# Kernel optimization log

Measured on AMD Instinct MI355X. Metric: run time of the kernel, lower is better.

The kernel has to match this reference:

```python
import jax, jax.numpy as jnp
import numpy as np

LN_EPS = 1e-5


def setup_inputs() -> dict:
    key = jax.random.key(0)
    ks = jax.random.split(key, 5)
    B, L, D, H = 4, 4096, 2048, 16
    s = 0.02  # keep activations in a sane range for fp32
    return {
        "x": jax.random.normal(ks[0], (B, L, D), jnp.float32),
        "Wq": jax.random.normal(ks[1], (D, D), jnp.float32) * s,
        "Wv": jax.random.normal(ks[2], (D, D), jnp.float32) * s,
        "Wg": jax.random.normal(ks[3], (D, D), jnp.float32) * s,
        "Wo": jax.random.normal(ks[4], (D, D), jnp.float32) * s,
        "beta": jnp.full((H,), -0.2, jnp.float32),  # module init: _beta = -0.2
        "ln_w": jnp.ones((D,), jnp.float32),
        "ln_b": jnp.zeros((D,), jnp.float32),
    }


def _retention_scan(v, lam):
    # v: (B, L, H, Dh); lam: (H,). state_t = lam * state_{t-1} + v_t
    B, L, H, Dh = v.shape
    a = jnp.broadcast_to(lam[None, None, :, None], (B, L, H, 1))

    def combine(c1, c2):
        a1, b1 = c1
        a2, b2 = c2
        return (a1 * a2, b1 * a2 + b2)

    _, state = jax.lax.associative_scan(combine, (a, v), axis=1)
    return state  # (B, L, H, Dh)


def reference(x, Wq, Wv, Wg, Wo, beta, ln_w, ln_b):
    B, L, D = x.shape
    H = beta.shape[0]
    Dh = D // H
    # bias-free projections (torch Linear: x @ W.T)
    q = (x @ Wq.T).reshape(B, L, H, Dh)
    v = (x @ Wv.T).reshape(B, L, H, Dh)
    lam = jax.nn.sigmoid(beta)  # per-head decay, (H,)
    state = _retention_scan(v, lam)  # decay-weighted cumulative sum
    y = (q * state).reshape(B, L, D)
    # LayerNorm over d_model
    mu = jnp.mean(y, axis=-1, keepdims=True)
    var = jnp.mean(jnp.square(y - mu), axis=-1, keepdims=True)
    y = (y - mu) * jax.lax.rsqrt(var + LN_EPS) * ln_w + ln_b
    # SiLU gate
    y = y * jax.nn.silu(x @ Wg.T)
    return y @ Wo.T
```

## Files before the change

kernel.cpp:

```cpp
#include <hip/hip_runtime.h>

#define BATCH 4
#define SEQ   4096
#define DMODEL 2048
#define NHEAD 16
#define DHEAD 128
#define MROWS (BATCH*SEQ)
#define LC    128
#define NCH   (SEQ/LC)

typedef unsigned short ushort_t;
typedef __bf16 v8bf __attribute__((ext_vector_type(8)));
typedef float  f32x4 __attribute__((ext_vector_type(4)));

__device__ __forceinline__ float b2f(ushort_t h) {
    return __uint_as_float(((unsigned)h) << 16);
}
__device__ __forceinline__ ushort_t f2b(float f) {
    unsigned u = __float_as_uint(f);
    return (ushort_t)((u + 0x7fffu + ((u >> 16) & 1u)) >> 16);
}

__global__ void cast_f32_bf16(const float* __restrict__ in, ushort_t* __restrict__ out, int n) {
    int i = (blockIdx.x * blockDim.x + threadIdx.x) * 8;
    const int stride = gridDim.x * blockDim.x * 8;
    for (; i < n; i += stride) {
        float4 a = *(const float4*)(in + i);
        float4 b = *(const float4*)(in + i + 4);
        ushort_t o[8] = {f2b(a.x), f2b(a.y), f2b(a.z), f2b(a.w),
                         f2b(b.x), f2b(b.y), f2b(b.z), f2b(b.w)};
        *(uint4*)(out + i) = *(const uint4*)o;
    }
}

__global__ void cast_weights(const float* __restrict__ w0, const float* __restrict__ w1,
                             const float* __restrict__ w2, const float* __restrict__ w3,
                             ushort_t* __restrict__ o0, ushort_t* __restrict__ o1,
                             ushort_t* __restrict__ o2, ushort_t* __restrict__ o3) {
    const int wsel = blockIdx.y;
    const float* src = wsel == 0 ? w0 : wsel == 1 ? w1 : wsel == 2 ? w2 : w3;
    ushort_t* dst    = wsel == 0 ? o0 : wsel == 1 ? o1 : wsel == 2 ? o2 : o3;
    const int n = DMODEL * DMODEL;
    int i = (blockIdx.x * blockDim.x + threadIdx.x) * 8;
    const int stride = gridDim.x * blockDim.x * 8;
    for (; i < n; i += stride) {
        float4 a = *(const float4*)(src + i);
        float4 b = *(const float4*)(src + i + 4);
        ushort_t o[8] = {f2b(a.x), f2b(a.y), f2b(a.z), f2b(a.w),
                         f2b(b.x), f2b(b.y), f2b(b.z), f2b(b.w)};
        *(uint4*)(dst + i) = *(const uint4*)o;
    }
}


#define GLL(src, dstoff) __builtin_amdgcn_global_load_lds( \
    (const __attribute__((address_space(1))) void*)(src), \
    (__attribute__((address_space(3))) void*)((char*)lds + (dstoff)), 16, 0, 0)

#define STG_A(buf, ks, kt) do { \
    GLL(gA0 + (kt) + (ks) * 32, (buf) * 65536 + (ks) * 16384 + dst0); \
    GLL(gA1 + (kt) + (ks) * 32, (buf) * 65536 + (ks) * 16384 + dst1); } while (0)
#define STG_B(buf, ks, kt) do { \
    GLL(gB0 + (kt) + (ks) * 32, (buf) * 65536 + 32768 + (ks) * 16384 + dst0); \
    GLL(gB1 + (kt) + (ks) * 32, (buf) * 65536 + 32768 + (ks) * 16384 + dst1); } while (0)

#define DSA(buf, ks, mh) do { \
    const ushort_t* _p = lds + (buf) * 32768 + (ks) * 8192 + abase + (mh) * 2048; \
    abuf[0] = *(const v8bf*)_p;          abuf[1] = *(const v8bf*)(_p + 512); \
    abuf[2] = *(const v8bf*)(_p + 1024); abuf[3] = *(const v8bf*)(_p + 1536); } while (0)
#define DSB(buf, ks) do { \
    const ushort_t* _p = lds + (buf) * 32768 + (ks) * 8192 + bbase; \
    bbuf[0] = *(const v8bf*)_p;          bbuf[1] = *(const v8bf*)(_p + 512); \
    bbuf[2] = *(const v8bf*)(_p + 1024); bbuf[3] = *(const v8bf*)(_p + 1536); } while (0)

#define VMW(n) asm volatile("s_waitcnt vmcnt(" #n ")" ::: "memory")
#define BAR()  __builtin_amdgcn_s_barrier()

#define MFMA_CORE(mh) do { \
    __builtin_amdgcn_s_barrier(); \
    asm volatile("s_waitcnt lgkmcnt(0)" ::: "memory"); \
    __builtin_amdgcn_sched_barrier(0); \
    __builtin_amdgcn_s_setprio(1); \
    _Pragma("unroll") \
    for (int _m = 0; _m < 4; ++_m) \
        _Pragma("unroll") \
        for (int _n = 0; _n < 4; ++_n) \
            acc[(mh) * 4 + _m][_n] = __builtin_amdgcn_mfma_f32_16x16x32_bf16( \
                abuf[_m], bbuf[_n], acc[(mh) * 4 + _m][_n], 0, 0, 0); \
    __builtin_amdgcn_s_setprio(0); \
    __builtin_amdgcn_sched_barrier(0); \
} while (0)

template<int N, int EPI>
__global__ __launch_bounds__(512, 2) void gemm8(const ushort_t* __restrict__ A,
                                                const ushort_t* __restrict__ Bm,
                                                ushort_t* __restrict__ o0,
                                                ushort_t* __restrict__ o1,
                                                ushort_t* __restrict__ o2,
                                                float* __restrict__ of) {
    constexpr int K  = DMODEL;
    constexpr int NT = K / 64;
    constexpr int NBN = N / 256;
    constexpr int NWG = (MROWS / 256) * NBN;
    extern __shared__ ushort_t lds[];

    int wg = blockIdx.x;
    wg = (wg & 7) * (NWG / 8) + (wg >> 3);
    const int tm = (wg / NBN) * 256;
    const int tn = (wg % NBN) * 256;

    const int tid  = threadIdx.x;
    const int lane = tid & 63;
    const int wid  = tid >> 6;
    const int wr   = wid >> 2;
    const int wc   = wid & 3;

    const int s0  = wid * 128 + lane;
    const int s1  = s0 + 64;
    const int r0s = s0 >> 2, r1s = s1 >> 2;
    const int c0s = (s0 & 3) ^ (r0s & 3) ^ ((r0s >> 2) & 3);
    const int c1s = (s1 & 3) ^ (r1s & 3) ^ ((r1s >> 2) & 3);
    const ushort_t* gA0 = A  + (size_t)(tm + r0s) * K + c0s * 8;
    const ushort_t* gA1 = A  + (size_t)(tm + r1s) * K + c1s * 8;
    const ushort_t* gB0 = Bm + (size_t)(tn + r0s) * K + c0s * 8;
    const ushort_t* gB1 = Bm + (size_t)(tn + r1s) * K + c1s * 8;
    const int dst0 = wid * 2048;
    const int dst1 = dst0 + 1024;

    const int l4    = lane & 15;
    const int c16p  = (lane >> 4) ^ (lane & 3) ^ ((lane >> 2) & 3);
    const int abase = (wr * 128 + l4) * 32 + c16p * 8;
    const int bbase = 16384 + (wc * 64 + l4) * 32 + c16p * 8;

    f32x4 acc[8][4] = {};
    v8bf abuf[4], bbuf[4];

    STG_A(0, 0, 0); STG_B(0, 0, 0); STG_A(0, 1, 0); STG_B(0, 1, 0);
    VMW(4);
    BAR();

    for (int t = 0; t < NT - 1; ++t) {
        const int cur = t & 1, nxt = cur ^ 1;
        const int ktn = (t + 1) * 64;
        STG_A(nxt, 0, ktn);
        DSA(cur, 0, 0); DSB(cur, 0);
        MFMA_CORE(0);
        BAR();
        STG_B(nxt, 0, ktn);
        DSA(cur, 0, 1);
        MFMA_CORE(1);
        VMW(4);
        BAR();
        STG_A(nxt, 1, ktn);
        DSA(cur, 1, 0); DSB(cur, 1);
        MFMA_CORE(0);
        BAR();
        STG_B(nxt, 1, ktn);
        DSA(cur, 1, 1);
        MFMA_CORE(1);
        VMW(4);
        BAR();
    }
    {
        const int cur = (NT - 1) & 1;
        DSA(cur, 0, 0); DSB(cur, 0);
        MFMA_CORE(0);
        BAR();
        DSA(cur, 0, 1);
        MFMA_CORE(1);
        VMW(0);
        BAR();
        DSA(cur, 1, 0); DSB(cur, 1);
        MFMA_CORE(0);
        BAR();
        DSA(cur, 1, 1);
        MFMA_CORE(1);
    }

    const int cr = (lane >> 4) * 4;
    const int cc = lane & 15;
    if constexpr (EPI == 0) {
        ushort_t* out = (tn < 2048) ? o0 : (tn < 4096 ? o1 : o2);
        const int nc0 = tn & 2047;
#pragma unroll
        for (int m = 0; m < 8; ++m) {
            const int r0 = tm + wr * 128 + m * 16 + cr;
#pragma unroll
            for (int n = 0; n < 4; ++n) {
                const int c = nc0 + wc * 64 + n * 16 + cc;
#pragma unroll
                for (int j = 0; j < 4; ++j)
                    out[(size_t)(r0 + j) * 2048 + c] = f2b(acc[m][n][j]);
            }
        }
    } else {
#pragma unroll
        for (int m = 0; m < 8; ++m) {
            const int r0 = tm + wr * 128 + m * 16 + cr;
#pragma unroll
            for (int n = 0; n < 4; ++n) {
                const int c = tn + wc * 64 + n * 16 + cc;
#pragma unroll
                for (int j = 0; j < 4; ++j)
                    of[(size_t)(r0 + j) * N + c] = acc[m][n][j];
            }
        }
    }
}

__global__ void scan_pass1(const ushort_t* __restrict__ v, const float* __restrict__ beta,
                           float* __restrict__ cf) {
    const int chunk = blockIdx.x, h = blockIdx.y, b = blockIdx.z;
    const int dh = threadIdx.x;
    const float lam = 1.f / (1.f + __expf(-beta[h]));
    size_t idx = ((size_t)(b * SEQ + chunk * LC) * NHEAD + h) * DHEAD + dh;
    float s = 0.f;
#pragma unroll 4
    for (int l = 0; l < LC; ++l) {
        s = fmaf(s, lam, b2f(v[idx]));
        idx += DMODEL;
    }
    cf[(((size_t)(b * NHEAD + h) * NCH) + chunk) * DHEAD + dh] = s;
}

__global__ void scan_pass2(float* __restrict__ cf, const float* __restrict__ beta) {
    const int t = blockIdx.x * blockDim.x + threadIdx.x;
    const int dh = t & 127;
    const int bh = t >> 7;
    const int h = bh & 15;
    const float lam = 1.f / (1.f + __expf(-beta[h]));
    float lamLc = lam;
#pragma unroll
    for (int i = 0; i < 7; ++i) lamLc *= lamLc;
    float carry = 0.f;
    for (int c = 0; c < NCH; ++c) {
        const size_t i = ((size_t)bh * NCH + c) * DHEAD + dh;
        const float val = cf[i];
        cf[i] = carry;
        carry = fmaf(carry, lamLc, val);
    }
}

__global__ void scan_pass3(const ushort_t* __restrict__ v, const ushort_t* __restrict__ q,
                           const float* __restrict__ beta, const float* __restrict__ cf,
                           ushort_t* __restrict__ y) {
    const int chunk = blockIdx.x, h = blockIdx.y, b = blockIdx.z;
    const int dh = threadIdx.x;
    const float lam = 1.f / (1.f + __expf(-beta[h]));
    float s = cf[(((size_t)(b * NHEAD + h) * NCH) + chunk) * DHEAD + dh];
    size_t idx = ((size_t)(b * SEQ + chunk * LC) * NHEAD + h) * DHEAD + dh;
#pragma unroll 4
    for (int l = 0; l < LC; ++l) {
        s = fmaf(s, lam, b2f(v[idx]));
        y[idx] = f2b(b2f(q[idx]) * s);
        idx += DMODEL;
    }
}

__global__ __launch_bounds__(256) void ln_gate(const ushort_t* __restrict__ y,
                                               const ushort_t* g,
                                               const float* __restrict__ lnw,
                                               const float* __restrict__ lnb,
                                               ushort_t* t) {
    const int row = blockIdx.x;
    const int tid = threadIdx.x;
    const size_t base = (size_t)row * DMODEL + tid * 8;

    float yv[8];
    {
        const uint4 raw = *(const uint4*)(y + base);
        const ushort_t* p = (const ushort_t*)&raw;
#pragma unroll
        for (int j = 0; j < 8; ++j) yv[j] = b2f(p[j]);
    }
    float s = 0.f, ss = 0.f;
#pragma unroll
    for (int j = 0; j < 8; ++j) { s += yv[j]; ss += yv[j] * yv[j]; }

#pragma unroll
    for (int o = 32; o > 0; o >>= 1) { s += __shfl_down(s, o); ss += __shfl_down(ss, o); }
    __shared__ float red[8];
    const int wid = tid >> 6, lane = tid & 63;
    if (lane == 0) { red[wid] = s; red[4 + wid] = ss; }
    __syncthreads();
    s  = red[0] + red[1] + red[2] + red[3];
    ss = red[4] + red[5] + red[6] + red[7];

    const float mu = s * (1.f / DMODEL);
    const float var = ss * (1.f / DMODEL) - mu * mu;
    const float rs = rsqrtf(var + 1e-5f);

    const int c0 = tid * 8;
    float4 w0 = *(const float4*)(lnw + c0), w1 = *(const float4*)(lnw + c0 + 4);
    float4 b0 = *(const float4*)(lnb + c0), b1 = *(const float4*)(lnb + c0 + 4);
    const float wv[8] = {w0.x, w0.y, w0.z, w0.w, w1.x, w1.y, w1.z, w1.w};
    const float bv[8] = {b0.x, b0.y, b0.z, b0.w, b1.x, b1.y, b1.z, b1.w};

    float gv[8];
    {
        const uint4 raw = *(const uint4*)(g + base);
        const ushort_t* p = (const ushort_t*)&raw;
#pragma unroll
        for (int j = 0; j < 8; ++j) gv[j] = b2f(p[j]);
    }

    ushort_t out[8];
#pragma unroll
    for (int j = 0; j < 8; ++j) {
        const float tv = (yv[j] - mu) * rs * wv[j] + bv[j];
        const float sil = gv[j] / (1.f + __expf(-gv[j]));
        out[j] = f2b(tv * sil);
    }
    *(uint4*)(t + base) = *(const uint4*)out;
}

#define OFF_XB  ((size_t)0)
#define OFF_WC  (OFF_XB + (size_t)MROWS*DMODEL*2)
#define OFF_WOB (OFF_WC + (size_t)3*DMODEL*DMODEL*2)
#define OFF_G   (OFF_WOB + (size_t)DMODEL*DMODEL*2)
#define OFF_CF  (OFF_G + (size_t)MROWS*DMODEL*2)
#define OFF_END (OFF_CF + (size_t)BATCH*NHEAD*NCH*DHEAD*4)

extern "C" void kernel_launch(void* const* d_in, const int* in_sizes, int n_in,
                              void* d_out, int out_size, void* d_ws, size_t ws_size,
                              hipStream_t stream) {
    if (ws_size < OFF_END) return;

    const float* x    = (const float*)d_in[0];
    const float* Wq   = (const float*)d_in[1];
    const float* Wv   = (const float*)d_in[2];
    const float* Wg   = (const float*)d_in[3];
    const float* Wo   = (const float*)d_in[4];
    const float* beta = (const float*)d_in[5];
    const float* lnw  = (const float*)d_in[6];
    const float* lnb  = (const float*)d_in[7];

    char* ws = (char*)d_ws;
    ushort_t* xb  = (ushort_t*)(ws + OFF_XB);
    ushort_t* Wc  = (ushort_t*)(ws + OFF_WC);
    ushort_t* Wob = (ushort_t*)(ws + OFF_WOB);
    ushort_t* g   = (ushort_t*)(ws + OFF_G);
    float*    cf  = (float*)(ws + OFF_CF);

    ushort_t* q = (ushort_t*)d_out;
    ushort_t* v = q + (size_t)MROWS * DMODEL;
    ushort_t* y = xb;
    ushort_t* t = g;

    const int DD = DMODEL * DMODEL;

    (void)hipFuncSetAttribute((const void*)gemm8<3 * DMODEL, 0>,
                              hipFuncAttributeMaxDynamicSharedMemorySize, 131072);
    (void)hipFuncSetAttribute((const void*)gemm8<DMODEL, 1>,
                              hipFuncAttributeMaxDynamicSharedMemorySize, 131072);

    cast_f32_bf16<<<2048, 256, 0, stream>>>(x, xb, MROWS * DMODEL);
    cast_weights<<<dim3(256, 4), 256, 0, stream>>>(Wq, Wv, Wg, Wo,
                                                   Wc, Wc + DD, Wc + 2 * DD, Wob);

    gemm8<3 * DMODEL, 0><<<(MROWS / 256) * (3 * DMODEL / 256), 512, 131072, stream>>>(
        xb, Wc, q, v, g, nullptr);

    scan_pass1<<<dim3(NCH, NHEAD, BATCH), DHEAD, 0, stream>>>(v, beta, cf);
    scan_pass2<<<(BATCH * NHEAD * DHEAD) / 256, 256, 0, stream>>>(cf, beta);
    scan_pass3<<<dim3(NCH, NHEAD, BATCH), DHEAD, 0, stream>>>(v, q, beta, cf, y);

    ln_gate<<<MROWS, 256, 0, stream>>>(y, g, lnw, lnb, t);

    gemm8<DMODEL, 1><<<(MROWS / 256) * (DMODEL / 256), 512, 131072, stream>>>(
        t, Wob, nullptr, nullptr, nullptr, (float*)d_out);
}
```

Baseline: 681.8 us.

## Restructure GEMM LDS layout to 64-wide rows and cut barriers per k-tile

Changes the LDS staging layout from two 32-column sub-slabs to full 64-column rows with an 8-way XOR swizzle, and rewrites the global-to-LDS load addressing to match. The main loop now waits on vmcnt and barriers once per k-tile at the start instead of at every MFMA quarter, which removes most workgroup barriers. Loads for the next buffer are issued between the four MFMA quarters. This relies on the vmcnt accounting being right for the double buffer, and it changes the bank-conflict pattern of the LDS reads.

```diff
diff --git a/kernel.cpp b/kernel.cpp
--- a/kernel.cpp
+++ b/kernel.cpp
@@ -57,27 +57,26 @@
     (const __attribute__((address_space(1))) void*)(src), \
     (__attribute__((address_space(3))) void*)((char*)lds + (dstoff)), 16, 0, 0)
 
-#define STG_A(buf, ks, kt) do { \
-    GLL(gA0 + (kt) + (ks) * 32, (buf) * 65536 + (ks) * 16384 + dst0); \
-    GLL(gA1 + (kt) + (ks) * 32, (buf) * 65536 + (ks) * 16384 + dst1); } while (0)
-#define STG_B(buf, ks, kt) do { \
-    GLL(gB0 + (kt) + (ks) * 32, (buf) * 65536 + 32768 + (ks) * 16384 + dst0); \
-    GLL(gB1 + (kt) + (ks) * 32, (buf) * 65536 + 32768 + (ks) * 16384 + dst1); } while (0)
-
-#define DSA(buf, ks, mh) do { \
-    const ushort_t* _p = lds + (buf) * 32768 + (ks) * 8192 + abase + (mh) * 2048; \
-    abuf[0] = *(const v8bf*)_p;          abuf[1] = *(const v8bf*)(_p + 512); \
-    abuf[2] = *(const v8bf*)(_p + 1024); abuf[3] = *(const v8bf*)(_p + 1536); } while (0)
-#define DSB(buf, ks) do { \
-    const ushort_t* _p = lds + (buf) * 32768 + (ks) * 8192 + bbase; \
-    bbuf[0] = *(const v8bf*)_p;          bbuf[1] = *(const v8bf*)(_p + 512); \
-    bbuf[2] = *(const v8bf*)(_p + 1024); bbuf[3] = *(const v8bf*)(_p + 1536); } while (0)
+#define STG_A(buf, half, kt) do { \
+    GLL(pA + ((half) * 128 +  0) * (size_t)K + (kt), (buf) * 65536 + (half) * 16384 + wid * 1024); \
+    GLL(pA + ((half) * 128 + 64) * (size_t)K + (kt), (buf) * 65536 + (half) * 16384 + wid * 1024 + 8192); } while (0)
+#define STG_B(buf, half, kt) do { \
+    GLL(pB + ((half) * 128 +  0) * (size_t)K + (kt), (buf) * 65536 + 32768 + (half) * 16384 + wid * 1024); \
+    GLL(pB + ((half) * 128 + 64) * (size_t)K + (kt), (buf) * 65536 + 32768 + (half) * 16384 + wid * 1024 + 8192); } while (0)
+
+#define DSA(buf, akk, mh) do { \
+    const ushort_t* _p = lds + (buf) * 32768 + (akk) + (mh) * 4096; \
+    abuf[0] = *(const v8bf*)_p;          abuf[1] = *(const v8bf*)(_p + 1024); \
+    abuf[2] = *(const v8bf*)(_p + 2048); abuf[3] = *(const v8bf*)(_p + 3072); } while (0)
+#define DSB(buf, bkk) do { \
+    const ushort_t* _p = lds + (buf) * 32768 + (bkk); \
+    bbuf[0] = *(const v8bf*)_p;          bbuf[1] = *(const v8bf*)(_p + 1024); \
+    bbuf[2] = *(const v8bf*)(_p + 2048); bbuf[3] = *(const v8bf*)(_p + 3072); } while (0)
 
 #define VMW(n) asm volatile("s_waitcnt vmcnt(" #n ")" ::: "memory")
 #define BAR()  __builtin_amdgcn_s_barrier()
 
-#define MFMA_CORE(mh) do { \
-    __builtin_amdgcn_s_barrier(); \
+#define MFMA_Q(mh) do { \
     asm volatile("s_waitcnt lgkmcnt(0)" ::: "memory"); \
     __builtin_amdgcn_sched_barrier(0); \
     __builtin_amdgcn_s_setprio(1); \
@@ -115,66 +114,55 @@
     const int wr   = wid >> 2;
     const int wc   = wid & 3;
 
-    const int s0  = wid * 128 + lane;
-    const int s1  = s0 + 64;
-    const int r0s = s0 >> 2, r1s = s1 >> 2;
-    const int c0s = (s0 & 3) ^ (r0s & 3) ^ ((r0s >> 2) & 3);
-    const int c1s = (s1 & 3) ^ (r1s & 3) ^ ((r1s >> 2) & 3);
-    const ushort_t* gA0 = A  + (size_t)(tm + r0s) * K + c0s * 8;
-    const ushort_t* gA1 = A  + (size_t)(tm + r1s) * K + c1s * 8;
-    const ushort_t* gB0 = Bm + (size_t)(tn + r0s) * K + c0s * 8;
-    const ushort_t* gB1 = Bm + (size_t)(tn + r1s) * K + c1s * 8;
-    const int dst0 = wid * 2048;
-    const int dst1 = dst0 + 1024;
-
-    const int l4    = lane & 15;
-    const int c16p  = (lane >> 4) ^ (lane & 3) ^ ((lane >> 2) & 3);
-    const int abase = (wr * 128 + l4) * 32 + c16p * 8;
-    const int bbase = 16384 + (wc * 64 + l4) * 32 + c16p * 8;
+    const int rs = wid * 8 + (lane >> 3);
+    const int cs = ((lane & 7) ^ ((lane >> 3) & 7)) * 8;
+    const ushort_t* pA = A  + (size_t)(tm + rs) * K + cs;
+    const ushort_t* pB = Bm + (size_t)(tn + rs) * K + cs;
+
+    const int q  = lane >> 4;
+    const int l4 = lane & 15;
+    const int sx = l4 & 7;
+    const int abase0 = (wr * 128 + l4) * 64 + ((q ^ sx)) * 8;
+    const int abase1 = (wr * 128 + l4) * 64 + (((4 + q) ^ sx)) * 8;
+    const int bbase0 = 16384 + (wc * 64 + l4) * 64 + ((q ^ sx)) * 8;
+    const int bbase1 = 16384 + (wc * 64 + l4) * 64 + (((4 + q) ^ sx)) * 8;
 
     f32x4 acc[8][4] = {};
     v8bf abuf[4], bbuf[4];
 
-    STG_A(0, 0, 0); STG_B(0, 0, 0); STG_A(0, 1, 0); STG_B(0, 1, 0);
-    VMW(4);
-    BAR();
+    STG_A(0, 0, 0); STG_A(0, 1, 0); STG_B(0, 0, 0); STG_B(0, 1, 0);
 
     for (int t = 0; t < NT - 1; ++t) {
         const int cur = t & 1, nxt = cur ^ 1;
         const int ktn = (t + 1) * 64;
         STG_A(nxt, 0, ktn);
-        DSA(cur, 0, 0); DSB(cur, 0);
-        MFMA_CORE(0);
+        VMW(2);
         BAR();
+        DSA(cur, abase0, 0); DSB(cur, bbase0);
+        MFMA_Q(0);
+        STG_A(nxt, 1, ktn);
+        DSA(cur, abase0, 1);
+        MFMA_Q(1);
         STG_B(nxt, 0, ktn);
-        DSA(cur, 0, 1);
-        MFMA_CORE(1);
-        VMW(4);
-        BAR();
-        STG_A(nxt, 1, ktn);
-        DSA(cur, 1, 0); DSB(cur, 1);
-        MFMA_CORE(0);
-        BAR();
+        DSA(cur, abase1, 0); DSB(cur, bbase1);
+        MFMA_Q(0);
         STG_B(nxt, 1, ktn);
-        DSA(cur, 1, 1);
-        MFMA_CORE(1);
-        VMW(4);
+        DSA(cur, abase1, 1);
+        MFMA_Q(1);
         BAR();
     }
     {
         const int cur = (NT - 1) & 1;
-        DSA(cur, 0, 0); DSB(cur, 0);
-        MFMA_CORE(0);
-        BAR();
-        DSA(cur, 0, 1);
-        MFMA_CORE(1);
         VMW(0);
         BAR();
-        DSA(cur, 1, 0); DSB(cur, 1);
-        MFMA_CORE(0);
-        BAR();
-        DSA(cur, 1, 1);
-        MFMA_CORE(1);
+        DSA(cur, abase0, 0); DSB(cur, bbase0);
+        MFMA_Q(0);
+        DSA(cur, abase0, 1);
+        MFMA_Q(1);
+        DSA(cur, abase1, 0); DSB(cur, bbase1);
+        MFMA_Q(0);
+        DSA(cur, abase1, 1);
+        MFMA_Q(1);
     }
 
     const int cr = (lane >> 4) * 4;
```

Result: faster. 640.0 us (-6.1%).
